# Kernel optimization log

Hardware: AMD Instinct MI355X
Metric: run time of the kernel (lower is better)

Reference implementation:

```python
import jax, jax.numpy as jnp
import numpy as np

T, B, F, P = 1024, 2048, 11, 256
KAPPA_MAX = 0.1
N_GRID = 100


def setup_inputs() -> dict:
    key = jax.random.key(0)
    k1, k2, k3, k4, k5 = jax.random.split(key, 5)
    aidx = jax.random.randint(k1, (T, B), 0, 2)
    actions = jax.nn.one_hot(aidx, 2, dtype=jnp.float32)            # (T,B,2) one-hot choice
    rewards = jax.random.bernoulli(k2, 0.5, (T, B, 2)).astype(jnp.float32)
    cd_cur = jax.random.uniform(k3, (T, B, 1), minval=-0.1, maxval=0.1)
    cd_next = jax.random.uniform(k4, (T, B, 1), minval=-0.1, maxval=0.1)
    meta = jnp.zeros((T, B, 4), dtype=jnp.float32)                  # timestep/trial/block/experiment (unused)
    pid = jax.random.randint(k5, (B,), 0, P).astype(jnp.float32)
    pid_feat = jnp.broadcast_to(pid[None, :, None], (T, B, 1))
    inputs = jnp.concatenate([actions, rewards, cd_cur, cd_next, meta, pid_feat], axis=-1)
    inputs = inputs[:, None]                                        # (T, 1, B, 11)
    return {
        "inputs": inputs,
        "beta_raw": jnp.zeros((P,), dtype=jnp.float32),
        "sigma_raw": jnp.zeros((P,), dtype=jnp.float32),
    }


def reference(inputs, beta_raw, sigma_raw):
    p_mu = jnp.linspace(0.0, 1.0, N_GRID)                           # (100,)
    x = jnp.nan_to_num(inputs[:, 0])                                # (T, B, 11)
    pid = x[0, :, -1].astype(jnp.int32)                             # (B,)
    beta = jnp.clip(jax.nn.softplus(beta_raw) + 1.0, 1.0, 25.0)[pid]    # (B,)
    sigma = jnp.clip(jax.nn.sigmoid(sigma_raw) * 0.09 + 0.01, 0.01, 0.1)[pid]  # (B,)
    inv_s = 1.0 / (sigma * jnp.sqrt(2.0))

    def ncdf(v, mean):
        return 0.5 * (1.0 + jax.lax.erf((v - mean) * inv_s))

    def state_beliefs(cd):
        u = ncdf(0.0, cd)
        v = ncdf(-KAPPA_MAX, cd)
        w = ncdf(KAPPA_MAX, cd)
        denom = jnp.maximum(w - v, 1e-10)
        pi_0 = jnp.clip((u - v) / denom, 0.0, 1.0)
        pi_1 = jnp.clip((w - u) / denom, 0.0, 1.0)
        return pi_0, pi_1

    def step(belief, x_t):
        acts = x_t[:, :2]
        rews = x_t[:, 2:4]
        cd_current = x_t[:, 4]
        cd_next = x_t[:, 5]
        had_choice = acts.sum(-1) > 0
        action_idx = jnp.argmax(acts, axis=-1)
        reward_scalar = (rews * acts).sum(-1)
        pi_0, pi_1 = state_beliefs(cd_current)
        r = jnp.where(action_idx == 0, reward_scalar, 1.0 - reward_scalar)
        q_0 = pi_1 * r + pi_0 * (1.0 - r)
        q_1 = (2.0 * r - 1.0) * (pi_0 - pi_1)
        update = q_1[:, None] * p_mu + q_0[:, None]                 # (B, 100)
        update = jnp.where(had_choice[:, None], update, 1.0)
        belief = jnp.maximum(belief * update, 1e-30)
        belief_norm = belief / belief.sum(-1, keepdims=True)
        E_mu = (belief_norm * p_mu).sum(-1)                         # (B,)
        pi_0n, pi_1n = state_beliefs(cd_next)
        v_a0 = (pi_0n - pi_1n) * E_mu + pi_1n
        v_a1 = (pi_1n - pi_0n) * E_mu + pi_0n
        logits_t = beta[:, None] * jnp.stack([v_a0, v_a1], axis=-1)  # (B, 2)
        return belief, logits_t

    belief0 = jnp.ones((x.shape[1], N_GRID), dtype=x.dtype)
    belief, logits = jax.lax.scan(step, belief0, x)                 # logits: (T, B, 2)
    logits = logits[:, None]                                        # (T, 1, B, 2)
    return logits, belief
```

## Files before the change

kernel.cpp:

```cpp
#include <hip/hip_runtime.h>
#include <math.h>

#define TT  1024
#define BB  2048
#define FF  11
#define PP  256
#define NG  100
#define NCH 32
#define LCH (TT / NCH)
#define JJ  4

typedef float f32x2 __attribute__((ext_vector_type(2)));
typedef float f32x4u __attribute__((ext_vector_type(4), aligned(4)));
typedef float f32x2u __attribute__((ext_vector_type(2), aligned(4)));

__device__ __forceinline__ float nz(float v) { return (v != v) ? 0.f : v; }

__device__ __forceinline__ float erf_fast(float x) {
    float ax = fabsf(x);
    float t  = __builtin_amdgcn_rcpf(fmaf(0.3275911f, ax, 1.f));
    float y  = fmaf(fmaf(fmaf(fmaf(1.061405429f, t, -1.453152027f), t,
                              1.421413741f), t, -0.284496736f), t, 0.254829592f);
    y *= t;
    float r = fmaf(-y, __expf(-ax * ax), 1.f);
    return copysignf(r, x);
}

__device__ __forceinline__ float4 q_from_rec(
    float a0, float a1, float r0, float r1, float cdc, float cdn,
    float beta, float inv_s)
{
    float u = 0.5f * (1.f + erf_fast((0.0f  - cdc) * inv_s));
    float v = 0.5f * (1.f + erf_fast((-0.1f - cdc) * inv_s));
    float w = 0.5f * (1.f + erf_fast((0.1f  - cdc) * inv_s));
    float inv = 1.f / fmaxf(w - v, 1e-10f);
    float pi0 = fminf(fmaxf((u - v) * inv, 0.f), 1.f);
    float pi1 = fminf(fmaxf((w - u) * inv, 0.f), 1.f);

    u = 0.5f * (1.f + erf_fast((0.0f  - cdn) * inv_s));
    v = 0.5f * (1.f + erf_fast((-0.1f - cdn) * inv_s));
    w = 0.5f * (1.f + erf_fast((0.1f  - cdn) * inv_s));
    inv = 1.f / fmaxf(w - v, 1e-10f);
    float pi0n = fminf(fmaxf((u - v) * inv, 0.f), 1.f);
    float pi1n = fminf(fmaxf((w - u) * inv, 0.f), 1.f);

    float rs = r0 * a0 + r1 * a1;
    float r  = (a0 >= a1) ? rs : 1.f - rs;
    float q0 = pi1 * r + pi0 * (1.f - r);
    float q1 = (2.f * r - 1.f) * (pi0 - pi1);
    if (!((a0 + a1) > 0.f)) { q0 = 1.f; q1 = 0.f; }
    return make_float4(q0, q1, beta * pi1n, beta * pi0n);
}

__global__ __launch_bounds__(256, 3) void phaseAq_kernel(
    const float* __restrict__ x, const float* __restrict__ beta_raw,
    const float* __restrict__ sigma_raw, float4* __restrict__ QC,
    float* __restrict__ UC)
{
    __shared__ float2 sq[4][4][64];
    const int lane = threadIdx.x & 63;
    const int wib  = threadIdx.x >> 6;
    const int W    = blockIdx.x * 4 + wib;
    const int wg   = W & 255;
    const int c    = W >> 8;
    const int g    = lane & 7;
    const int sl   = lane >> 3;
    const int b    = wg * 8 + g;
    const int t0   = c * LCH;

    f32x4u r4[4];
    f32x2u r2[4];
    #pragma unroll
    for (int r = 0; r < 4; ++r) {
        const float* rec = x + (size_t)(t0 + 8 * r + sl) * (BB * FF) + b * FF;
        r4[r] = *(const f32x4u*)rec;
        r2[r] = *(const f32x2u*)(rec + 4);
    }

    int pid = (int)nz(x[(size_t)b * FF + 10]);
    pid = pid < 0 ? 0 : (pid > PP - 1 ? PP - 1 : pid);
    float br = beta_raw[pid];
    float sr = sigma_raw[pid];
    float sp   = fmaxf(br, 0.f) + log1pf(__expf(-fabsf(br)));
    float beta = fminf(fmaxf(sp + 1.f, 1.f), 25.f);
    float sig  = fminf(fmaxf(__builtin_amdgcn_rcpf(1.f + __expf(-sr)) * 0.09f + 0.01f,
                             0.01f), 0.1f);
    float inv_s = 1.f / (sig * 1.41421356237309505f);

    f32x2 p[7];
    #pragma unroll
    for (int k = 0; k < 7; ++k)
        p[k] = (f32x2){ (float)(sl + 16 * k)     * (1.f / 99.f),
                        (float)(sl + 16 * k + 8) * (1.f / 99.f) };

    #pragma unroll
    for (int r = 0; r < 4; ++r) {
        float a0 = nz(r4[r].x), a1 = nz(r4[r].y), r0 = nz(r4[r].z),
              r1 = nz(r4[r].w), dc = nz(r2[r].x), dn = nz(r2[r].y);
        float4 qc = q_from_rec(a0, a1, r0, r1, dc, dn, beta, inv_s);
        QC[(size_t)(t0 + 8 * r + sl) * BB + b] = qc;
        sq[wib][r][sl * 8 + g] = make_float2(qc.x, qc.y);
    }
    __builtin_amdgcn_wave_barrier();

    f32x2 U[4][7];
    #pragma unroll
    for (int r = 0; r < 4; ++r)
        #pragma unroll
        for (int k = 0; k < 7; ++k) U[r][k] = (f32x2){1.f, 1.f};

    #pragma unroll
    for (int j = 0; j < 8; ++j) {
        #pragma unroll
        for (int r = 0; r < 4; ++r) {
            float2 qj = sq[wib][r][j * 8 + g];
            f32x2 qx = { qj.x, qj.x }, qy = { qj.y, qj.y };
            #pragma unroll
            for (int k = 0; k < 7; ++k) {
                f32x2 u = qy * p[k] + qx;
                U[r][k] *= u;
            }
        }
    }

    float* dst = UC + (size_t)c * (NG * BB) + b;
    #pragma unroll
    for (int k = 0; k < 7; ++k) {
        f32x2 Uf = ((U[0][k] * U[1][k]) * U[2][k]) * U[3][k];
        if (k < 6) {
            dst[(size_t)(sl + 16 * k) * BB]     = Uf.x;
            dst[(size_t)(sl + 16 * k + 8) * BB] = Uf.y;
        } else if (sl < 4) {
            dst[(size_t)(sl + 96) * BB] = Uf.x;
        }
    }
}

__global__ __launch_bounds__(256) void phaseB_kernel(
    const float* __restrict__ UC, float* __restrict__ BE)
{
    const int flat = blockIdx.x * 256 + threadIdx.x;
    float be = 1.f;
    #pragma unroll
    for (int c = 0; c < NCH; ++c) {
        BE[(size_t)c * (BB * NG) + flat] = be;
        float u = UC[(size_t)c * (BB * NG) + flat];
        be = fmaxf(be * u, 1e-30f);
    }
}

__global__ __launch_bounds__(256) void phaseC_kernel(
    const float4* __restrict__ QC, const float* __restrict__ BE,
    float* __restrict__ out)
{
    const int lane = threadIdx.x & 63;
    const int wib  = threadIdx.x >> 6;
    const int W    = blockIdx.x * 4 + wib;
    const int wg   = W & 255;
    const int c    = W >> 8;
    const int sl   = lane & 7;
    const int g    = lane >> 3;
    const int b    = wg * 8 + g;
    const int t0   = c * LCH;

    f32x2 p[7];
    #pragma unroll
    for (int k = 0; k < 7; ++k)
        p[k] = (f32x2){ (float)(sl + 16 * k)     * (1.f / 99.f),
                        (float)(sl + 16 * k + 8) * (1.f / 99.f) };
    const f32x2 clA = { 1e-30f, 1e-30f };
    const f32x2 cl6 = { (sl < 4) ? 1e-30f : 0.f, 0.f };

    const float* ebase = BE + (size_t)c * (BB * NG) + b;
    f32x2 be[7];
    #pragma unroll
    for (int k = 0; k < 6; ++k)
        be[k] = (f32x2){ ebase[(size_t)(sl + 16 * k) * BB],
                         ebase[(size_t)(sl + 16 * k + 8) * BB] };
    be[6] = (f32x2){ (sl < 4) ? ebase[(size_t)(sl + 96) * BB] : 0.f, 0.f };

    const char* QCb = (const char*)QC;
    char* outb = (char*)out;
    unsigned off  = ((unsigned)t0 * BB + (unsigned)b) * 16u;
    unsigned soff = ((unsigned)t0 * (2 * BB) + 2 * (unsigned)b) * 4u;

    float4 pre[JJ];
    #pragma unroll
    for (int j = 0; j < JJ; ++j)
        pre[j] = *(const float4*)(QCb + (off + (unsigned)j * (BB * 16u)));
    off += JJ * (BB * 16u);

    for (int tt = 0; tt < LCH; tt += JJ) {
        float S[JJ], Sp[JJ], Zv[JJ], Wv[JJ];
        #pragma unroll
        for (int j = 0; j < JJ; ++j) {
            float4 q = pre[j];
            pre[j] = *(const float4*)(QCb + (off + (unsigned)j * (BB * 16u)));
            f32x2 qx = { q.x, q.x }, qy = { q.y, q.y };
            #pragma unroll
            for (int k = 0; k < 7; ++k) {
                f32x2 u = qy * p[k] + qx;
                be[k] = __builtin_elementwise_max(be[k] * u,
                                                  (k == 6) ? cl6 : clA);
            }
            f32x2 sA = ((be[0] + be[1]) + (be[2] + be[3]))
                     + ((be[4] + be[5]) + be[6]);
            S[j] = sA.x + sA.y;
            f32x2 a1 = be[0] * p[0], a2 = be[1] * p[1];
            a1 = be[2] * p[2] + a1;  a2 = be[3] * p[3] + a2;
            a1 = be[4] * p[4] + a1;  a2 = be[5] * p[5] + a2;
            a1 = be[6] * p[6] + a1;
            f32x2 aa = a1 + a2;
            Sp[j] = aa.x + aa.y;
            Zv[j] = q.z;
            Wv[j] = q.w;
        }
        off += JJ * (BB * 16u);
        #pragma unroll
        for (int j = 0; j < JJ; ++j) {
            float st = S[j], sr = Sp[j];
            {
                int t;
                t = __builtin_amdgcn_update_dpp(0, __float_as_int(st), 0xB1, 0xF, 0xF, true);
                st += __int_as_float(t);
                t = __builtin_amdgcn_update_dpp(0, __float_as_int(sr), 0xB1, 0xF, 0xF, true);
                sr += __int_as_float(t);
                t = __builtin_amdgcn_update_dpp(0, __float_as_int(st), 0x4E, 0xF, 0xF, true);
                st += __int_as_float(t);
                t = __builtin_amdgcn_update_dpp(0, __float_as_int(sr), 0x4E, 0xF, 0xF, true);
                sr += __int_as_float(t);
                t = __builtin_amdgcn_update_dpp(0, __float_as_int(st), 0x141, 0xF, 0xF, true);
                st += __int_as_float(t);
                t = __builtin_amdgcn_update_dpp(0, __float_as_int(sr), 0x141, 0xF, 0xF, true);
                sr += __int_as_float(t);
            }
            float E  = sr * __builtin_amdgcn_rcpf(st);
            float A  = Wv[j] - Zv[j];
            float l0 = fmaf(A, E, Zv[j]);
            float l1 = fmaf(-A, E, Wv[j]);
            if (sl == 0)
                *(float2*)(outb + (soff + (unsigned)j * (2 * BB * 4u))) =
                    make_float2(l0, l1);
        }
        soff += JJ * (2 * BB * 4u);
    }

    if (c == NCH - 1) {
        float* bel = out + (size_t)TT * BB * 2 + (size_t)b * NG;
        #pragma unroll
        for (int k = 0; k < 6; ++k) {
            bel[sl + 16 * k]     = be[k].x;
            bel[sl + 16 * k + 8] = be[k].y;
        }
        if (sl < 4) bel[sl + 96] = be[6].x;
    }
}

extern "C" void kernel_launch(void* const* d_in, const int* in_sizes, int n_in,
                              void* d_out, int out_size, void* d_ws, size_t ws_size,
                              hipStream_t stream)
{
    const float* x         = (const float*)d_in[0];
    const float* beta_raw  = (const float*)d_in[1];
    const float* sigma_raw = (const float*)d_in[2];
    float* out = (float*)d_out;

    char* ws = (char*)d_ws;
    float4* QC = (float4*)ws;
    float*  UC = (float*)(ws + (size_t)TT * BB * 16);
    float*  BE = (float*)(ws + (size_t)TT * BB * 16 + (size_t)NCH * BB * NG * 4);

    phaseAq_kernel<<<(BB / 8) * NCH / 4, 256, 0, stream>>>(x, beta_raw, sigma_raw, QC, UC);
    phaseB_kernel<<<(BB * NG) / 256, 256, 0, stream>>>(UC, BE);
    phaseC_kernel<<<(BB / 8) * NCH / 4, 256, 0, stream>>>(QC, BE, out);
}
```

Before: 196.0 us.

## Recompute per-step coefficients in phase C instead of storing QC buffer

Phase A no longer writes the per-timestep float4 coefficient array to global memory. Phase C instead rereads the raw input records and recomputes the coefficients with the erf-based belief math, then stages them through shared memory in half-chunk tiles. This removes a 32 MB write and its later read, paid for with duplicated transcendental work and a reread of the input in phase C. Phase C also gets a launch-bounds occupancy hint.

```diff
diff --git a/kernel.cpp b/kernel.cpp
--- a/kernel.cpp
+++ b/kernel.cpp
@@ -8,7 +8,6 @@
 #define NG  100
 #define NCH 32
 #define LCH (TT / NCH)
-#define JJ  4
 
 typedef float f32x2 __attribute__((ext_vector_type(2)));
 typedef float f32x4u __attribute__((ext_vector_type(4), aligned(4)));
@@ -52,10 +51,24 @@
     return make_float4(q0, q1, beta * pi1n, beta * pi0n);
 }
 
+__device__ __forceinline__ float2 participant(
+    const float* __restrict__ x, const float* __restrict__ beta_raw,
+    const float* __restrict__ sigma_raw, int b)
+{
+    int pid = (int)nz(x[(size_t)b * FF + 10]);
+    pid = pid < 0 ? 0 : (pid > PP - 1 ? PP - 1 : pid);
+    float br = beta_raw[pid];
+    float sr = sigma_raw[pid];
+    float sp   = fmaxf(br, 0.f) + log1pf(__expf(-fabsf(br)));
+    float beta = fminf(fmaxf(sp + 1.f, 1.f), 25.f);
+    float sig  = fminf(fmaxf(__builtin_amdgcn_rcpf(1.f + __expf(-sr)) * 0.09f + 0.01f,
+                             0.01f), 0.1f);
+    return make_float2(beta, 1.f / (sig * 1.41421356237309505f));
+}
+
 __global__ __launch_bounds__(256, 3) void phaseAq_kernel(
     const float* __restrict__ x, const float* __restrict__ beta_raw,
-    const float* __restrict__ sigma_raw, float4* __restrict__ QC,
-    float* __restrict__ UC)
+    const float* __restrict__ sigma_raw, float* __restrict__ UC)
 {
     __shared__ float2 sq[4][4][64];
     const int lane = threadIdx.x & 63;
@@ -77,15 +90,8 @@
         r2[r] = *(const f32x2u*)(rec + 4);
     }
 
-    int pid = (int)nz(x[(size_t)b * FF + 10]);
-    pid = pid < 0 ? 0 : (pid > PP - 1 ? PP - 1 : pid);
-    float br = beta_raw[pid];
-    float sr = sigma_raw[pid];
-    float sp   = fmaxf(br, 0.f) + log1pf(__expf(-fabsf(br)));
-    float beta = fminf(fmaxf(sp + 1.f, 1.f), 25.f);
-    float sig  = fminf(fmaxf(__builtin_amdgcn_rcpf(1.f + __expf(-sr)) * 0.09f + 0.01f,
-                             0.01f), 0.1f);
-    float inv_s = 1.f / (sig * 1.41421356237309505f);
+    const float2 pr = participant(x, beta_raw, sigma_raw, b);
+    const float beta = pr.x, inv_s = pr.y;
 
     f32x2 p[7];
     #pragma unroll
@@ -98,7 +104,6 @@
         float a0 = nz(r4[r].x), a1 = nz(r4[r].y), r0 = nz(r4[r].z),
               r1 = nz(r4[r].w), dc = nz(r2[r].x), dn = nz(r2[r].y);
         float4 qc = q_from_rec(a0, a1, r0, r1, dc, dn, beta, inv_s);
-        QC[(size_t)(t0 + 8 * r + sl) * BB + b] = qc;
         sq[wib][r][sl * 8 + g] = make_float2(qc.x, qc.y);
     }
     __builtin_amdgcn_wave_barrier();
@@ -149,10 +154,12 @@
     }
 }
 
-__global__ __launch_bounds__(256) void phaseC_kernel(
-    const float4* __restrict__ QC, const float* __restrict__ BE,
+__global__ __launch_bounds__(256, 3) void phaseC_kernel(
+    const float* __restrict__ x, const float* __restrict__ beta_raw,
+    const float* __restrict__ sigma_raw, const float* __restrict__ BE,
     float* __restrict__ out)
 {
+    __shared__ float4 tile[4][16][8];
     const int lane = threadIdx.x & 63;
     const int wib  = threadIdx.x >> 6;
     const int W    = blockIdx.x * 4 + wib;
@@ -161,12 +168,27 @@
     const int sl   = lane & 7;
     const int g    = lane >> 3;
     const int b    = wg * 8 + g;
+    const int g1   = lane & 7;
+    const int sl1  = lane >> 3;
+    const int b1   = wg * 8 + g1;
     const int t0   = c * LCH;
 
-    f32x2 p[7];
+    f32x4u r4[4];
+    f32x2u r2[4];
+    #pragma unroll
+    for (int r = 0; r < 4; ++r) {
+        const float* rec = x + (size_t)(t0 + 8 * r + sl1) * (BB * FF) + b1 * FF;
+        r4[r] = *(const f32x4u*)rec;
+        r2[r] = *(const f32x2u*)(rec + 4);
+    }
+
+    const float2 pr = participant(x, beta_raw, sigma_raw, b1);
+    const float beta = pr.x, inv_s = pr.y;
+
+    f32x2 p3[7];
     #pragma unroll
     for (int k = 0; k < 7; ++k)
-        p[k] = (f32x2){ (float)(sl + 16 * k)     * (1.f / 99.f),
+        p3[k] = (f32x2){ (float)(sl + 16 * k)     * (1.f / 99.f),
                         (float)(sl + 16 * k + 8) * (1.f / 99.f) };
     const f32x2 clA = { 1e-30f, 1e-30f };
     const f32x2 cl6 = { (sl < 4) ? 1e-30f : 0.f, 0.f };
@@ -179,70 +201,74 @@
                          ebase[(size_t)(sl + 16 * k + 8) * BB] };
     be[6] = (f32x2){ (sl < 4) ? ebase[(size_t)(sl + 96) * BB] : 0.f, 0.f };
 
-    const char* QCb = (const char*)QC;
-    char* outb = (char*)out;
-    unsigned off  = ((unsigned)t0 * BB + (unsigned)b) * 16u;
-    unsigned soff = ((unsigned)t0 * (2 * BB) + 2 * (unsigned)b) * 4u;
-
-    float4 pre[JJ];
-    #pragma unroll
-    for (int j = 0; j < JJ; ++j)
-        pre[j] = *(const float4*)(QCb + (off + (unsigned)j * (BB * 16u)));
-    off += JJ * (BB * 16u);
-
-    for (int tt = 0; tt < LCH; tt += JJ) {
-        float S[JJ], Sp[JJ], Zv[JJ], Wv[JJ];
+    #pragma unroll
+    for (int half = 0; half < 2; ++half) {
         #pragma unroll
-        for (int j = 0; j < JJ; ++j) {
-            float4 q = pre[j];
-            pre[j] = *(const float4*)(QCb + (off + (unsigned)j * (BB * 16u)));
-            f32x2 qx = { q.x, q.x }, qy = { q.y, q.y };
+        for (int r = 0; r < 2; ++r) {
+            const int rr = 2 * half + r;
+            float a0 = nz(r4[rr].x), a1 = nz(r4[rr].y), r0 = nz(r4[rr].z),
+                  r1 = nz(r4[rr].w), dc = nz(r2[rr].x), dn = nz(r2[rr].y);
+            float4 qc = q_from_rec(a0, a1, r0, r1, dc, dn, beta, inv_s);
+            tile[wib][8 * r + sl1][g1] = qc;
+        }
+        __builtin_amdgcn_wave_barrier();
+
+        for (int tt = 0; tt < 16; tt += 4) {
+            float S[4], Sp[4], Zv[4], Wv[4];
+            float4 q4[4];
             #pragma unroll
-            for (int k = 0; k < 7; ++k) {
-                f32x2 u = qy * p[k] + qx;
-                be[k] = __builtin_elementwise_max(be[k] * u,
-                                                  (k == 6) ? cl6 : clA);
+            for (int j = 0; j < 4; ++j)
+                q4[j] = tile[wib][tt + j][g];
+            #pragma unroll
+            for (int j = 0; j < 4; ++j) {
+                float4 qf = q4[j];
+                f32x2 qx = { qf.x, qf.x }, qy = { qf.y, qf.y };
+                #pragma unroll
+                for (int k = 0; k < 7; ++k) {
+                    f32x2 u = qy * p3[k] + qx;
+                    be[k] = __builtin_elementwise_max(be[k] * u,
+                                                      (k == 6) ? cl6 : clA);
+                }
+                f32x2 sA = ((be[0] + be[1]) + (be[2] + be[3]))
+                         + ((be[4] + be[5]) + be[6]);
+                S[j] = sA.x + sA.y;
+                f32x2 a1v = be[0] * p3[0], a2v = be[1] * p3[1];
+                a1v = be[2] * p3[2] + a1v;  a2v = be[3] * p3[3] + a2v;
+                a1v = be[4] * p3[4] + a1v;  a2v = be[5] * p3[5] + a2v;
+                a1v = be[6] * p3[6] + a1v;
+                f32x2 aa = a1v + a2v;
+                Sp[j] = aa.x + aa.y;
+                Zv[j] = qf.z;
+                Wv[j] = qf.w;
             }
-            f32x2 sA = ((be[0] + be[1]) + (be[2] + be[3]))
-                     + ((be[4] + be[5]) + be[6]);
-            S[j] = sA.x + sA.y;
-            f32x2 a1 = be[0] * p[0], a2 = be[1] * p[1];
-            a1 = be[2] * p[2] + a1;  a2 = be[3] * p[3] + a2;
-            a1 = be[4] * p[4] + a1;  a2 = be[5] * p[5] + a2;
-            a1 = be[6] * p[6] + a1;
-            f32x2 aa = a1 + a2;
-            Sp[j] = aa.x + aa.y;
-            Zv[j] = q.z;
-            Wv[j] = q.w;
-        }
-        off += JJ * (BB * 16u);
-        #pragma unroll
-        for (int j = 0; j < JJ; ++j) {
-            float st = S[j], sr = Sp[j];
-            {
-                int t;
-                t = __builtin_amdgcn_update_dpp(0, __float_as_int(st), 0xB1, 0xF, 0xF, true);
-                st += __int_as_float(t);
-                t = __builtin_amdgcn_update_dpp(0, __float_as_int(sr), 0xB1, 0xF, 0xF, true);
-                sr += __int_as_float(t);
-                t = __builtin_amdgcn_update_dpp(0, __float_as_int(st), 0x4E, 0xF, 0xF, true);
-                st += __int_as_float(t);
-                t = __builtin_amdgcn_update_dpp(0, __float_as_int(sr), 0x4E, 0xF, 0xF, true);
-                sr += __int_as_float(t);
-                t = __builtin_amdgcn_update_dpp(0, __float_as_int(st), 0x141, 0xF, 0xF, true);
-                st += __int_as_float(t);
-                t = __builtin_amdgcn_update_dpp(0, __float_as_int(sr), 0x141, 0xF, 0xF, true);
-                sr += __int_as_float(t);
+            #pragma unroll
+            for (int j = 0; j < 4; ++j) {
+                float st = S[j], sr = Sp[j];
+                {
+                    int t;
+                    t = __builtin_amdgcn_update_dpp(0, __float_as_int(st), 0xB1, 0xF, 0xF, true);
+                    st += __int_as_float(t);
+                    t = __builtin_amdgcn_update_dpp(0, __float_as_int(sr), 0xB1, 0xF, 0xF, true);
+                    sr += __int_as_float(t);
+                    t = __builtin_amdgcn_update_dpp(0, __float_as_int(st), 0x4E, 0xF, 0xF, true);
+                    st += __int_as_float(t);
+                    t = __builtin_amdgcn_update_dpp(0, __float_as_int(sr), 0x4E, 0xF, 0xF, true);
+                    sr += __int_as_float(t);
+                    t = __builtin_amdgcn_update_dpp(0, __float_as_int(st), 0x141, 0xF, 0xF, true);
+                    st += __int_as_float(t);
+                    t = __builtin_amdgcn_update_dpp(0, __float_as_int(sr), 0x141, 0xF, 0xF, true);
+                    sr += __int_as_float(t);
+                }
+                float E  = sr * __builtin_amdgcn_rcpf(st);
+                float A  = Wv[j] - Zv[j];
+                float l0 = fmaf(A, E, Zv[j]);
+                float l1 = fmaf(-A, E, Wv[j]);
+                if (sl == 0)
+                    *(float2*)(out + (size_t)(t0 + 16 * half + tt + j) * (2 * BB) + 2 * b) =
+                        make_float2(l0, l1);
             }
-            float E  = sr * __builtin_amdgcn_rcpf(st);
-            float A  = Wv[j] - Zv[j];
-            float l0 = fmaf(A, E, Zv[j]);
-            float l1 = fmaf(-A, E, Wv[j]);
-            if (sl == 0)
-                *(float2*)(outb + (soff + (unsigned)j * (2 * BB * 4u))) =
-                    make_float2(l0, l1);
-        }
-        soff += JJ * (2 * BB * 4u);
+        }
+        __builtin_amdgcn_wave_barrier();
     }
 
     if (c == NCH - 1) {
@@ -266,11 +292,10 @@
     float* out = (float*)d_out;
 
     char* ws = (char*)d_ws;
-    float4* QC = (float4*)ws;
-    float*  UC = (float*)(ws + (size_t)TT * BB * 16);
-    float*  BE = (float*)(ws + (size_t)TT * BB * 16 + (size_t)NCH * BB * NG * 4);
-
-    phaseAq_kernel<<<(BB / 8) * NCH / 4, 256, 0, stream>>>(x, beta_raw, sigma_raw, QC, UC);
+    float*  UC = (float*)ws;
+    float*  BE = (float*)(ws + (size_t)NCH * BB * NG * 4);
+
+    phaseAq_kernel<<<(BB / 8) * NCH / 4, 256, 0, stream>>>(x, beta_raw, sigma_raw, UC);
     phaseB_kernel<<<(BB * NG) / 256, 256, 0, stream>>>(UC, BE);
-    phaseC_kernel<<<(BB / 8) * NCH / 4, 256, 0, stream>>>(QC, BE, out);
-}
+    phaseC_kernel<<<(BB / 8) * NCH / 4, 256, 0, stream>>>(x, beta_raw, sigma_raw, BE, out);
+}
```

Result: slower. 200.6 us (+2.4%).

## Fuse chunk prefix-product into phase C by recomputing from chunk products

Applied to the files above, without the earlier changes.

Removes the separate prefix-product kernel and its BE buffer; each phase C wave now multiplies together all preceding chunk update products from UC to get its starting belief. This saves a kernel launch and a full write plus reread of the prefix buffer. In exchange, later chunks perform redundant serial reads over all previous chunks, giving quadratic total UC traffic and load imbalance across waves.

```diff
diff --git a/kernel.cpp b/kernel.cpp
--- a/kernel.cpp
+++ b/kernel.cpp
@@ -136,21 +136,8 @@
     }
 }
 
-__global__ __launch_bounds__(256) void phaseB_kernel(
-    const float* __restrict__ UC, float* __restrict__ BE)
-{
-    const int flat = blockIdx.x * 256 + threadIdx.x;
-    float be = 1.f;
-    #pragma unroll
-    for (int c = 0; c < NCH; ++c) {
-        BE[(size_t)c * (BB * NG) + flat] = be;
-        float u = UC[(size_t)c * (BB * NG) + flat];
-        be = fmaxf(be * u, 1e-30f);
-    }
-}
-
 __global__ __launch_bounds__(256) void phaseC_kernel(
-    const float4* __restrict__ QC, const float* __restrict__ BE,
+    const float4* __restrict__ QC, const float* __restrict__ UC,
     float* __restrict__ out)
 {
     const int lane = threadIdx.x & 63;
@@ -171,13 +158,24 @@
     const f32x2 clA = { 1e-30f, 1e-30f };
     const f32x2 cl6 = { (sl < 4) ? 1e-30f : 0.f, 0.f };
 
-    const float* ebase = BE + (size_t)c * (BB * NG) + b;
     f32x2 be[7];
     #pragma unroll
-    for (int k = 0; k < 6; ++k)
-        be[k] = (f32x2){ ebase[(size_t)(sl + 16 * k) * BB],
-                         ebase[(size_t)(sl + 16 * k + 8) * BB] };
-    be[6] = (f32x2){ (sl < 4) ? ebase[(size_t)(sl + 96) * BB] : 0.f, 0.f };
+    for (int k = 0; k < 6; ++k) be[k] = (f32x2){1.f, 1.f};
+    be[6] = (f32x2){ (sl < 4) ? 1.f : 0.f, 0.f };
+    {
+        const float* ub = UC + b;
+        for (int cc = 0; cc < c; ++cc) {
+            const float* ucc = ub + (size_t)cc * (NG * BB);
+            #pragma unroll
+            for (int k = 0; k < 6; ++k) {
+                f32x2 uu = { ucc[(size_t)(sl + 16 * k) * BB],
+                             ucc[(size_t)(sl + 16 * k + 8) * BB] };
+                be[k] = __builtin_elementwise_max(be[k] * uu, clA);
+            }
+            f32x2 u6 = { (sl < 4) ? ucc[(size_t)(sl + 96) * BB] : 1.f, 1.f };
+            be[6] = __builtin_elementwise_max(be[6] * u6, cl6);
+        }
+    }
 
     const char* QCb = (const char*)QC;
     char* outb = (char*)out;
@@ -268,9 +266,7 @@
     char* ws = (char*)d_ws;
     float4* QC = (float4*)ws;
     float*  UC = (float*)(ws + (size_t)TT * BB * 16);
-    float*  BE = (float*)(ws + (size_t)TT * BB * 16 + (size_t)NCH * BB * NG * 4);
 
     phaseAq_kernel<<<(BB / 8) * NCH / 4, 256, 0, stream>>>(x, beta_raw, sigma_raw, QC, UC);
-    phaseB_kernel<<<(BB * NG) / 256, 256, 0, stream>>>(UC, BE);
-    phaseC_kernel<<<(BB / 8) * NCH / 4, 256, 0, stream>>>(QC, BE, out);
-}
+    phaseC_kernel<<<(BB / 8) * NCH / 4, 256, 0, stream>>>(QC, UC, out);
+}
```

Measured after the change: 266.1 us. +35.8%, slower.
